# Kernel optimization log

Measured on AMD Instinct MI355X. Metric: run time of the kernel, lower is better.

Reference implementation:

```python
import jax, jax.numpy as jnp
import numpy as np

EMBED = 1024
HEADS = 16
HEAD_DIM = EMBED // HEADS  # 64 quantum wires


def setup_inputs() -> dict:
    key = jax.random.key(0)
    ks = jax.random.split(key, 6)
    s = 1.0 / np.sqrt(EMBED)
    return {
        "x": jax.random.normal(ks[0], (8, 4096, EMBED), dtype=jnp.float32),
        "Wk": jax.random.normal(ks[1], (EMBED, EMBED), dtype=jnp.float32) * s,
        "Wq": jax.random.normal(ks[2], (EMBED, EMBED), dtype=jnp.float32) * s,
        "Wv": jax.random.normal(ks[3], (EMBED, EMBED), dtype=jnp.float32) * s,
        "Wo": jax.random.normal(ks[4], (EMBED, EMBED), dtype=jnp.float32) * s,
        "theta": jax.random.normal(ks[5], (HEAD_DIM,), dtype=jnp.float32),
    }


def reference(x, Wk, Wq, Wv, Wo, theta):
    b, s, _ = x.shape
    # linear projections (torch Linear: y = x @ W^T), split heads -> [b,s,h,d]
    def proj(W):
        return (x @ W.T).reshape(b, s, HEADS, HEAD_DIM)
    k, q, v = proj(Wk), proj(Wq), proj(Wv)
    # QLayer: per-wire RX(x_i) then trainable RX(theta_i) on |0>, measure PauliZ
    # -> <Z_i> = cos(x_i + theta_i) exactly (product state, independent wires).
    k_q = jnp.cos(k + theta)
    q_q = jnp.cos(q + theta)
    v_q = jnp.cos(v + theta)
    # Faithful to source: matmul over last two dims of [b,s,h,d] -> attention
    # across the HEADS axis ([b,s,h,h]), not across sequence.
    scores = jnp.einsum('bsid,bsjd->bsij', q_q, k_q) / jnp.sqrt(
        jnp.asarray(HEAD_DIM, dtype=x.dtype))
    attn = jax.nn.softmax(scores, axis=-1)  # dropout = identity at inference
    out = jnp.einsum('bsij,bsjd->bsid', attn, v_q).reshape(b, s, EMBED)
    return out @ Wo.T
```

## Files before the change

kernel.cpp:

```cpp
#include <hip/hip_runtime.h>
#include <hip/hip_fp16.h>

#define NTOK 32768
#define NE   1024

typedef _Float16 half_t;
typedef _Float16 f16x8 __attribute__((ext_vector_type(8)));
typedef _Float16 f16x4 __attribute__((ext_vector_type(4)));
typedef float    f32x4 __attribute__((ext_vector_type(4)));

typedef __attribute__((address_space(1))) const unsigned int guint;
typedef __attribute__((address_space(3))) unsigned int luint;

__device__ __forceinline__ void async16(const void* g, void* l) {
    __builtin_amdgcn_global_load_lds((guint*)g, (luint*)l, 16, 0, 0);
}

__global__ __launch_bounds__(256) void cvt_all(const float* __restrict__ x,
                                               const float* __restrict__ w0,
                                               const float* __restrict__ w1,
                                               const float* __restrict__ w2,
                                               const float* __restrict__ w3,
                                               half_t* __restrict__ dx,
                                               half_t* __restrict__ dw) {
    const int id = blockIdx.x;
    const float* s;
    half_t* d;
    int i;
    if (id < 16384) {
        s = x; d = dx;
        i = (id * 256 + threadIdx.x) * 8;
    } else {
        const int m = (id - 16384) >> 9;
        const float* ws[4] = {w0, w1, w2, w3};
        s = ws[m];
        d = dw + (size_t)m * (NE * NE);
        i = (((id - 16384) & 511) * 256 + threadIdx.x) * 8;
    }
    float4 a = *(const float4*)(s + i);
    float4 b = *(const float4*)(s + i + 4);
    f16x8 h = {(_Float16)a.x, (_Float16)a.y, (_Float16)a.z, (_Float16)a.w,
               (_Float16)b.x, (_Float16)b.y, (_Float16)b.z, (_Float16)b.w};
    *(f16x8*)(d + i) = h;
}


#define WAITV(N) asm volatile("s_waitcnt vmcnt(" #N ")" ::: "memory")
#define BARRIER()                              \
    do {                                       \
        asm volatile("" ::: "memory");         \
        __builtin_amdgcn_s_barrier();          \
        asm volatile("" ::: "memory");         \
    } while (0)

#define ASC(b, c) (Asm + ((b) * 2 + (c)) * 8192)
#define BSC(b, c) (Bsm + ((b) * 2 + (c)) * 8192)

#define STAGE_A(dst, q, k0)                                                   \
    do {                                                                      \
        _Pragma("unroll") for (int l = 0; l < 2; ++l)                         \
            async16(Ag + (size_t)(l * 128 + (q) * 64 + rr) * K + (k0) + cc,   \
                    (char*)(dst) + l * 8192 + w * 1024);                      \
    } while (0)

#define STAGE_B(dst, r, k0)                                                   \
    do {                                                                      \
        _Pragma("unroll") for (int l = 0; l < 2; ++l)                         \
            async16(Bg + (size_t)((l * 2 + wb) * 64 + (r) * 32 + (rr & 31)) * K + \
                        (k0) + cc,                                            \
                    (char*)(dst) + l * 8192 + w * 1024);                      \
    } while (0)

#define READ_A(dstf, b, q)                                                    \
    do {                                                                      \
        _Pragma("unroll") for (int i = 0; i < 4; ++i)                         \
        _Pragma("unroll") for (int x = 0; x < 2; ++x)                         \
            dstf[i][x] = *(const f16x8*)&ASC(b, q)[(wr * 64 + i * 16 + l16) * 64 + \
                                                   (((x * 4 + quad) ^ sw) * 8)]; \
    } while (0)

#define READ_B(dstf, b, r)                                                    \
    do {                                                                      \
        _Pragma("unroll") for (int i2 = 0; i2 < 2; ++i2)                      \
        _Pragma("unroll") for (int x = 0; x < 2; ++x)                         \
            dstf[i2][x] = *(const f16x8*)&BSC(b, r)[(wc * 32 + i2 * 16 + l16) * 64 + \
                                                    (((x * 4 + quad) ^ sw) * 8)]; \
    } while (0)

#define MMA(af, bf, QA, RB)                                                   \
    do {                                                                      \
        __builtin_amdgcn_s_setprio(1);                                        \
        _Pragma("unroll") for (int i = 0; i < 4; ++i)                         \
        _Pragma("unroll") for (int jj = 0; jj < 2; ++jj)                      \
        _Pragma("unroll") for (int x = 0; x < 2; ++x)                         \
            acc[(QA) * 4 + i][(RB) * 2 + jj] =                                \
                __builtin_amdgcn_mfma_f32_16x16x32_f16(                       \
                    af[i][x], bf[jj][x], acc[(QA) * 4 + i][(RB) * 2 + jj], 0, 0, 0); \
        __builtin_amdgcn_s_setprio(0);                                        \
    } while (0)

template <bool QKV>
__global__ __launch_bounds__(512, 2) void gemm_bt(const half_t* __restrict__ A,
                                                  const half_t* __restrict__ Bbase,
                                                  void* __restrict__ Cout,
                                                  const float* __restrict__ theta) {
    constexpr int K  = 1024;
    constexpr int NT = 16;
    constexpr int J  = QKV ? 12 : 4;
    __shared__ alignas(16) half_t smem[65536];
    half_t* Asm = smem;
    half_t* Bsm = smem + 32768;

    const int id    = blockIdx.x;
    const int xcd   = id & 7;
    const int slot  = id >> 3;
    const int ygrp  = slot / J;
    const int j     = slot - ygrp * J;
    const int mtile = ygrp * 8 + xcd;
    const int zsl   = QKV ? (j >> 2) : 0;
    const int xt    = QKV ? (j & 3) : j;

    const int tid  = threadIdx.x;
    const int w    = tid >> 6;
    const int lane = tid & 63;
    const int quad = lane >> 4;
    const int l16  = lane & 15;
    const int sw   = l16 & 7;
    const int wr   = w >> 2, wc = w & 3;
    const size_t m0 = (size_t)mtile * 256;
    const int    n0 = xt * 256;

    const half_t* Ag = A + m0 * K;
    const half_t* Bg = Bbase + (size_t)zsl * (size_t)(NE * NE) + (size_t)n0 * K;

    const int rr = tid >> 3;
    const int cc = ((tid & 7) ^ (rr & 7)) * 8;
    const int wb = tid >> 8;

    f32x4 acc[8][4];
#pragma unroll
    for (int i = 0; i < 8; ++i)
#pragma unroll
        for (int jj = 0; jj < 4; ++jj) acc[i][jj] = (f32x4){0.f, 0.f, 0.f, 0.f};

    STAGE_A(ASC(0, 0), 0, 0);
    STAGE_B(BSC(0, 0), 0, 0);
    STAGE_B(BSC(0, 1), 1, 0);
    STAGE_A(ASC(0, 1), 1, 0);
    STAGE_A(ASC(1, 0), 0, 64);
    WAITV(6);
    BARRIER();

    f16x8 aF0[4][2], aF1[4][2], bF0[2][2], bF1[2][2];
    READ_A(aF0, 0, 0);
    READ_B(bF0, 0, 0);

#pragma unroll 1
    for (int t = 0; t < NT - 1; ++t) {
        const int cur = t & 1, nxt = cur ^ 1;
        const int kn = (t + 1) * 64;
        WAITV(4);
        BARRIER();
        STAGE_B(BSC(nxt, 0), 0, kn);
        MMA(aF0, bF0, 0, 0);
        READ_B(bF1, cur, 1);
        WAITV(4);
        BARRIER();
        STAGE_B(BSC(nxt, 1), 1, kn);
        MMA(aF0, bF1, 0, 1);
        READ_A(aF1, cur, 1);
        STAGE_A(ASC(nxt, 1), 1, kn);
        MMA(aF1, bF1, 1, 1);
        WAITV(4);
        BARRIER();
        if (t + 2 < NT) STAGE_A(ASC(cur, 0), 0, kn + 64);
        MMA(aF1, bF0, 1, 0);
        READ_A(aF0, nxt, 0);
        READ_B(bF0, nxt, 0);
    }
    {
        WAITV(2);
        BARRIER();
        MMA(aF0, bF0, 0, 0);
        READ_B(bF1, 1, 1);
        WAITV(0);
        BARRIER();
        MMA(aF0, bF1, 0, 1);
        READ_A(aF1, 1, 1);
        MMA(aF1, bF1, 1, 1);
        MMA(aF1, bF0, 1, 0);
    }
    __syncthreads();

    if (QKV) {
        half_t* Cl = smem;
#pragma unroll
        for (int nt = 0; nt < 4; ++nt) {
            const int col = wc * 64 + nt * 16 + l16;
            const float th = theta[col & 63];
#pragma unroll
            for (int mt = 0; mt < 8; ++mt) {
                const int rowb = wr * 128 + mt * 16 + quad * 4;
#pragma unroll
                for (int r = 0; r < 4; ++r) {
                    const int row = rowb + r;
                    Cl[row * 256 + (col ^ (((row >> 2) & 3) << 4))] =
                        (half_t)__cosf(acc[mt][nt][r] + th);
                }
            }
        }
        __syncthreads();
        half_t* Cg = (half_t*)Cout + (size_t)zsl * ((size_t)NTOK * NE);
#pragma unroll
        for (int it = 0; it < 16; ++it) {
            const int row = it * 16 + (tid >> 5);
            const int seg = tid & 31;
            f16x8 vv = *(const f16x8*)&Cl[row * 256 +
                                          ((seg * 8) ^ (((row >> 2) & 3) << 4))];
            *(f16x8*)&Cg[(m0 + row) * NE + n0 + seg * 8] = vv;
        }
    } else {
        float* ClF = (float*)smem;
        float* Cg  = (float*)Cout;
#pragma unroll
        for (int s = 0; s < 2; ++s) {
            if (wr == s) {
#pragma unroll
                for (int nt = 0; nt < 4; ++nt) {
                    const int col = wc * 64 + nt * 16 + l16;
#pragma unroll
                    for (int mt = 0; mt < 8; ++mt) {
                        const int rowb = mt * 16 + quad * 4;
#pragma unroll
                        for (int r = 0; r < 4; ++r) {
                            const int row = rowb + r;
                            ClF[row * 256 + (col ^ (((row >> 2) & 1) << 4))] =
                                acc[mt][nt][r];
                        }
                    }
                }
            }
            __syncthreads();
#pragma unroll
            for (int it = 0; it < 16; ++it) {
                const int row = it * 8 + (tid >> 6);
                const int seg = tid & 63;
                f32x4 vv = *(const f32x4*)&ClF[row * 256 +
                                               ((seg * 4) ^ (((row >> 2) & 1) << 4))];
                *(f32x4*)&Cg[(m0 + s * 128 + row) * NE + n0 + seg * 4] = vv;
            }
            __syncthreads();
        }
    }
}

__global__ __launch_bounds__(512) void attn_kernel(const half_t* __restrict__ q,
                                                   const half_t* __restrict__ k,
                                                   const half_t* __restrict__ v,
                                                   half_t* __restrict__ out) {
    __shared__ half_t vT[8][64][20];
    __shared__ half_t Pl[8][16][20];
    const int tid  = threadIdx.x;
    const int w    = tid >> 6;
    const int lane = tid & 63;
    const int quad = lane >> 4;
    const int l16  = lane & 15;
    const size_t base = ((size_t)blockIdx.x * 8 + w) * 1024;

    {
        const int h = lane >> 2, d0 = (lane & 3) * 16;
        f16x8 va = *(const f16x8*)(v + base + h * 64 + d0);
        f16x8 vb = *(const f16x8*)(v + base + h * 64 + d0 + 8);
#pragma unroll
        for (int z = 0; z < 8; ++z) {
            vT[w][d0 + z][h]     = va[z];
            vT[w][d0 + 8 + z][h] = vb[z];
        }
    }

    f16x8 aq0 = *(const f16x8*)(q + base + l16 * 64 + quad * 8);
    f16x8 aq1 = *(const f16x8*)(q + base + l16 * 64 + 32 + quad * 8);
    f16x8 bk0 = *(const f16x8*)(k + base + l16 * 64 + quad * 8);
    f16x8 bk1 = *(const f16x8*)(k + base + l16 * 64 + 32 + quad * 8);
    f32x4 S = __builtin_amdgcn_mfma_f32_16x16x32_f16(aq0, bk0, (f32x4){0.f,0.f,0.f,0.f}, 0, 0, 0);
    S = __builtin_amdgcn_mfma_f32_16x16x32_f16(aq1, bk1, S, 0, 0, 0);

#pragma unroll
    for (int r = 0; r < 4; ++r) {
        float s = S[r] * 0.125f;
        float mx = s;
#pragma unroll
        for (int o = 8; o; o >>= 1) mx = fmaxf(mx, __shfl_xor(mx, o));
        float e = __expf(s - mx);
        float sum = e;
#pragma unroll
        for (int o = 8; o; o >>= 1) sum += __shfl_xor(sum, o);
        Pl[w][quad * 4 + r][l16] = (half_t)(e / sum);
    }
    __syncthreads();

    f16x4 ap = *(const f16x4*)&Pl[w][l16][quad * 4];
#pragma unroll
    for (int c = 0; c < 4; ++c) {
        f16x4 bv = *(const f16x4*)&vT[w][c * 16 + l16][quad * 4];
        f32x4 O = __builtin_amdgcn_mfma_f32_16x16x16f16(ap, bv, (f32x4){0.f,0.f,0.f,0.f}, 0, 0, 0);
#pragma unroll
        for (int r = 0; r < 4; ++r)
            out[base + (quad * 4 + r) * 64 + c * 16 + l16] = (half_t)O[r];
    }
}

extern "C" void kernel_launch(void* const* d_in, const int* in_sizes, int n_in,
                              void* d_out, int out_size, void* d_ws, size_t ws_size,
                              hipStream_t stream) {
    const float* x     = (const float*)d_in[0];
    const float* Wk    = (const float*)d_in[1];
    const float* Wq    = (const float*)d_in[2];
    const float* Wv    = (const float*)d_in[3];
    const float* Wo    = (const float*)d_in[4];
    const float* theta = (const float*)d_in[5];

    char* ws = (char*)d_ws;
    half_t* xh  = (half_t*)ws;
    half_t* wh  = (half_t*)(ws + (size_t)(64 << 20));
    half_t* qkv = (half_t*)(ws + (size_t)(72 << 20));

    cvt_all<<<16384 + 4 * 512, 256, 0, stream>>>(x, Wq, Wk, Wv, Wo, xh, wh);

    gemm_bt<true><<<1536, 512, 0, stream>>>(xh, wh, qkv, theta);

    attn_kernel<<<NTOK / 8, 512, 0, stream>>>(qkv, qkv + (size_t)NTOK * NE,
                                              qkv + 2 * (size_t)NTOK * NE, xh);

    gemm_bt<false><<<512, 512, 0, stream>>>(xh, wh + 3 * NE * NE, d_out, nullptr);
}
```

Measured before the change: 550.3 us.

## Deepen GEMM pipeline to prefetch two K-tiles ahead with fewer barriers

Restructures the fp16 MFMA GEMM main loop so global-to-LDS async loads run two K-steps ahead instead of one, prefetching a full second buffer in the prologue. Barriers are cut from three to two per iteration, plus an LDS-read-completion barrier (lgkmcnt wait). The epilogue is split into two explicit final steps. This hides more global load latency and reduces synchronisation stalls, at the cost of more outstanding loads and a tighter buffer-reuse ordering that must stay correct.

Result: slower. 571.7 us (+3.9%).

```diff
diff --git a/kernel.cpp b/kernel.cpp
--- a/kernel.cpp
+++ b/kernel.cpp
@@ -52,6 +52,12 @@
         __builtin_amdgcn_s_barrier();          \
         asm volatile("" ::: "memory");         \
     } while (0)
+#define BARL()                                             \
+    do {                                                   \
+        asm volatile("s_waitcnt lgkmcnt(0)" ::: "memory"); \
+        __builtin_amdgcn_s_barrier();                      \
+        asm volatile("" ::: "memory");                     \
+    } while (0)
 
 #define ASC(b, c) (Asm + ((b) * 2 + (c)) * 8192)
 #define BSC(b, c) (Bsm + ((b) * 2 + (c)) * 8192)
@@ -105,7 +111,6 @@
                                                   void* __restrict__ Cout,
                                                   const float* __restrict__ theta) {
     constexpr int K  = 1024;
-    constexpr int NT = 16;
     constexpr int J  = QKV ? 12 : 4;
     __shared__ alignas(16) half_t smem[65536];
     half_t* Asm = smem;
@@ -148,43 +153,53 @@
     STAGE_B(BSC(0, 1), 1, 0);
     STAGE_A(ASC(0, 1), 1, 0);
     STAGE_A(ASC(1, 0), 0, 64);
-    WAITV(6);
+    STAGE_B(BSC(1, 0), 0, 64);
+    STAGE_B(BSC(1, 1), 1, 64);
+    STAGE_A(ASC(1, 1), 1, 64);
+    WAITV(8);
     BARRIER();
 
     f16x8 aF0[4][2], aF1[4][2], bF0[2][2], bF1[2][2];
     READ_A(aF0, 0, 0);
     READ_B(bF0, 0, 0);
+    BARL();
 
 #pragma unroll 1
-    for (int t = 0; t < NT - 1; ++t) {
+    for (int t = 0; t < 14; ++t) {
         const int cur = t & 1, nxt = cur ^ 1;
-        const int kn = (t + 1) * 64;
-        WAITV(4);
-        BARRIER();
-        STAGE_B(BSC(nxt, 0), 0, kn);
+        const int kf = (t + 2) * 64;
+        STAGE_A(ASC(cur, 0), 0, kf);
+        STAGE_B(BSC(cur, 0), 0, kf);
         MMA(aF0, bF0, 0, 0);
         READ_B(bF1, cur, 1);
-        WAITV(4);
-        BARRIER();
-        STAGE_B(BSC(nxt, 1), 1, kn);
         MMA(aF0, bF1, 0, 1);
         READ_A(aF1, cur, 1);
-        STAGE_A(ASC(nxt, 1), 1, kn);
+        BARL();
+        STAGE_B(BSC(cur, 1), 1, kf);
+        STAGE_A(ASC(cur, 1), 1, kf);
         MMA(aF1, bF1, 1, 1);
-        WAITV(4);
+        MMA(aF1, bF0, 1, 0);
+        WAITV(8);
         BARRIER();
-        if (t + 2 < NT) STAGE_A(ASC(cur, 0), 0, kn + 64);
-        MMA(aF1, bF0, 1, 0);
         READ_A(aF0, nxt, 0);
         READ_B(bF0, nxt, 0);
+        BARL();
     }
     {
-        WAITV(2);
+        MMA(aF0, bF0, 0, 0);
+        READ_B(bF1, 0, 1);
+        MMA(aF0, bF1, 0, 1);
+        READ_A(aF1, 0, 1);
+        MMA(aF1, bF1, 1, 1);
+        MMA(aF1, bF0, 1, 0);
+        WAITV(0);
         BARRIER();
+        READ_A(aF0, 1, 0);
+        READ_B(bF0, 1, 0);
+    }
+    {
         MMA(aF0, bF0, 0, 0);
         READ_B(bF1, 1, 1);
-        WAITV(0);
-        BARRIER();
         MMA(aF0, bF1, 0, 1);
         READ_A(aF1, 1, 1);
         MMA(aF1, bF1, 1, 1);
```
